# Optimization experiments

Measured on AMD Instinct MI355X. Metric: run time of the kernel, lower is better.

## Reference

```python
import jax, jax.numpy as jnp
import numpy as np

NUM_ITERATIONS = 3


def squash(s):
    # s: [..., out_channels]; norm over last axis (matches torch squash on squeezed tensor)
    norm = jnp.linalg.norm(s, axis=-1, keepdims=True)
    return (norm ** 2 / (1.0 + norm ** 2)) * (s / norm)


def setup_inputs() -> dict:
    key = jax.random.key(0)
    k1, k2 = jax.random.split(key)
    B, R, C, O, I = 256, 192, 96, 16, 20
    x = jax.random.normal(k1, (B, R, I), dtype=jnp.float32)
    W = jax.random.normal(k2, (R, C, O, I), dtype=jnp.float32)
    return {"x": x, "W": W}


def reference(x, W):
    # u_hat[b,r,c,o] = W[r,c,o,i] @ x[b,r,i]  (torch: matmul(W, x[i]) per batch element)
    u_hat = jnp.einsum('rcoi,bri->brco', W, x)  # [B,R,C,O]
    R, C = W.shape[0], W.shape[1]
    b_ij = jnp.zeros((R, C), dtype=x.dtype)  # shared across batch (torch b_ij is [1,R,C,1])
    v_j = None
    for it in range(NUM_ITERATIONS):
        c_ij = jax.nn.softmax(b_ij, axis=0)                 # softmax over routes (dim=1 in torch)
        s_j = jnp.einsum('rc,brco->bco', c_ij, u_hat)        # weighted sum over routes
        v_j = squash(s_j)                                    # [B,C,O]
        if it < NUM_ITERATIONS - 1:
            # agreement: <u_hat, v_j> averaged over batch (torch mean(dim=0))
            a_ij = jnp.einsum('brco,bco->rc', u_hat, v_j) / x.shape[0]
            b_ij = b_ij + a_ij
    return v_j  # [B, num_capsules, out_channels] (torch returns trailing singleton [B,C,O,1])
```

## Files before the change

kernel.cpp:

```cpp
#include <hip/hip_runtime.h>


#define R_ 192
#define C_ 96
#define O_ 16
#define I_ 20
#define B_ 256
#define K1 3840
#define N_ 1536
#define ZSPLIT 20
#define STILE 393216

typedef unsigned short u16;
typedef __attribute__((ext_vector_type(8))) short short8;
typedef __attribute__((ext_vector_type(4))) float floatx4;

__device__ inline float bf2f(u16 h) {
  union { unsigned int u; float f; } x; x.u = ((unsigned int)h) << 16; return x.f;
}
__device__ inline u16 f2bf(float f) {
  union { float f; unsigned int u; } x; x.f = f;
  unsigned int r = x.u + 0x7FFFu + ((x.u >> 16) & 1u);
  return (u16)(r >> 16);
}
__device__ inline unsigned int pack2(float a, float b) {
  return (unsigned int)f2bf(a) | ((unsigned int)f2bf(b) << 16);
}

__global__ void k_prep(const float* __restrict__ W, const float* __restrict__ X,
                       u16* __restrict__ WtT, u16* __restrict__ Xk,
                       u16* __restrict__ xT, float* __restrict__ bij) {
  int bid = blockIdx.x;
  if (bid < 23040) {
    int t = bid * 256 + threadIdx.x;
    int n = t / K1, k = t - n * K1;
    int c = n >> 4, o = n & 15;
    int r = k / I_, i = k - r * I_;
    WtT[t] = f2bf(W[(((r * C_ + c) * O_ + o) * I_) + i]);
  } else if (bid < 23280) {
    __shared__ u16 tile[64][72];
    int idx = bid - 23040;
    int kb = (idx % 60) << 6, bb = (idx / 60) << 6;
    int brow = threadIdx.x >> 4;
    int kq = (threadIdx.x & 15) << 2;
    #pragma unroll
    for (int p = 0; p < 4; ++p) {
      int bl = p * 16 + brow;
      float4 v = *(const float4*)(X + (size_t)(bb + bl) * K1 + kb + kq);
      ushort4 h;
      h.x = f2bf(v.x); h.y = f2bf(v.y); h.z = f2bf(v.z); h.w = f2bf(v.w);
      *(ushort4*)(Xk + (size_t)(bb + bl) * K1 + kb + kq) = h;
      tile[kq + 0][bl] = h.x;
      tile[kq + 1][bl] = h.y;
      tile[kq + 2][bl] = h.z;
      tile[kq + 3][bl] = h.w;
    }
    __syncthreads();
    int kr = threadIdx.x >> 3;
    int bq = (threadIdx.x & 7) << 3;
    #pragma unroll
    for (int q = 0; q < 2; ++q) {
      int kl = q * 32 + kr;
      *(uint4*)(xT + (size_t)(kb + kl) * B_ + bb + bq) = *(const uint4*)&tile[kl][bq];
    }
  } else {
    int t = (bid - 23280) * 256 + threadIdx.x;
    bij[t] = 0.0f;
  }
}

__device__ inline uint4 scale_b8(uint4 raw, int kg, const float* smrow) {
  int r0 = kg / I_;
  int bnd = (r0 + 1) * I_ - kg;
  float s0 = smrow[r0];
  float s1 = smrow[(r0 + 1 < R_) ? r0 + 1 : R_ - 1];
  union { uint4 q; u16 h[8]; } u; u.q = raw;
  #pragma unroll
  for (int j = 0; j < 8; ++j)
    u.h[j] = f2bf(bf2f(u.h[j]) * ((j < bnd) ? s0 : s1));
  return u.q;
}

__global__ __launch_bounds__(256) void gemm1(
    const u16* __restrict__ A, const u16* __restrict__ Bt,
    const float* __restrict__ bij, u16* __restrict__ P,
    int kChunk, int kIters) {
  const int K = K1;
  __shared__ u16 As[128 * 32];
  __shared__ u16 Bs[128 * 32];
  __shared__ float sm[8][192];
  int tid = threadIdx.x;
  {
    int cg = tid >> 5, lr = tid & 31;
    int c = (blockIdx.y << 3) + cg;
    float e[6]; float mx = -1e30f;
    #pragma unroll
    for (int j = 0; j < 6; ++j) {
      e[j] = bij[(lr + (j << 5)) * C_ + c];
      mx = fmaxf(mx, e[j]);
    }
    #pragma unroll
    for (int off = 16; off > 0; off >>= 1) mx = fmaxf(mx, __shfl_xor(mx, off));
    float sum = 0.f;
    #pragma unroll
    for (int j = 0; j < 6; ++j) { e[j] = expf(e[j] - mx); sum += e[j]; }
    #pragma unroll
    for (int off = 16; off > 0; off >>= 1) sum += __shfl_xor(sum, off);
    float inv = 1.0f / sum;
    #pragma unroll
    for (int j = 0; j < 6; ++j) sm[cg][lr + (j << 5)] = e[j] * inv;
  }
  __syncthreads();

  long m0 = (long)blockIdx.x * 128, n0 = (long)blockIdx.y * 128;
  int k0 = blockIdx.z * kChunk;
  const u16* Ab = A + m0 * K + k0;
  const u16* Bb = Bt + n0 * K + k0;
  int srow = tid >> 2;
  int scol = (tid & 3) << 3;
  int w = tid >> 6, lane = tid & 63;
  int wm = (w >> 1) << 6, wn = (w & 1) << 6;
  int quad = lane >> 4, lrow = lane & 15;
  int cl0 = srow >> 4;
  floatx4 acc[4][4];
  #pragma unroll
  for (int a = 0; a < 4; ++a)
    #pragma unroll
    for (int b = 0; b < 4; ++b) acc[a][b] = (floatx4){0.f, 0.f, 0.f, 0.f};

  for (int kt = 0; kt < kIters; ++kt) {
    int kk = kt << 5;
    uint4 a0 = *(const uint4*)(Ab + (long)srow * K + kk + scol);
    uint4 a1 = *(const uint4*)(Ab + (long)(srow + 64) * K + kk + scol);
    uint4 b0 = *(const uint4*)(Bb + (long)srow * K + kk + scol);
    uint4 b1 = *(const uint4*)(Bb + (long)(srow + 64) * K + kk + scol);
    int kg = k0 + kk + scol;
    uint4 b0s = scale_b8(b0, kg, &sm[cl0][0]);
    uint4 b1s = scale_b8(b1, kg, &sm[cl0 + 4][0]);
    __syncthreads();
    ((uint4*)As)[tid] = a0;
    ((uint4*)As)[tid + 256] = a1;
    ((uint4*)Bs)[tid] = b0s;
    ((uint4*)Bs)[tid + 256] = b1s;
    __syncthreads();
    short8 af[4], bfr[4];
    #pragma unroll
    for (int ms = 0; ms < 4; ++ms)
      af[ms] = *(const short8*)&As[(wm + ms * 16 + lrow) * 32 + (quad << 3)];
    #pragma unroll
    for (int ns = 0; ns < 4; ++ns)
      bfr[ns] = *(const short8*)&Bs[(wn + ns * 16 + lrow) * 32 + (quad << 3)];
    #pragma unroll
    for (int ms = 0; ms < 4; ++ms)
      #pragma unroll
      for (int ns = 0; ns < 4; ++ns)
        acc[ms][ns] = __builtin_amdgcn_mfma_f32_16x16x32_bf16(
            af[ms], bfr[ns], acc[ms][ns], 0, 0, 0);
  }
  size_t zb = (size_t)blockIdx.z * (size_t)STILE;
  #pragma unroll
  for (int ms = 0; ms < 4; ++ms)
    #pragma unroll
    for (int ns = 0; ns < 4; ++ns) {
      int b = (int)m0 + wm + ms * 16 + (quad << 2);
      int n = (int)n0 + wn + ns * 16 + lrow;
      uint2 pk;
      pk.x = pack2(acc[ms][ns][0], acc[ms][ns][1]);
      pk.y = pack2(acc[ms][ns][2], acc[ms][ns][3]);
      *(uint2*)&P[zb + (size_t)n * B_ + b] = pk;
    }
}

__global__ __launch_bounds__(256) void gemm2_agree(
    const u16* __restrict__ A, const u16* __restrict__ Bt,
    const u16* __restrict__ WtT, float* __restrict__ bij) {
  const int K = 256;
  __shared__ u16 As[128 * 32];
  __shared__ u16 Bs[128 * 32];
  int tid = threadIdx.x;
  long m0 = (long)blockIdx.x * 128, n0 = (long)blockIdx.y * 128;
  int k0 = blockIdx.z << 7;
  const u16* Ab = A + m0 * K + k0;
  const u16* Bb = Bt + n0 * K + k0;
  int srow = tid >> 2;
  int scol = (tid & 3) << 3;
  int w = tid >> 6, lane = tid & 63;
  int wm = (w >> 1) << 6, wn = (w & 1) << 6;
  int quad = lane >> 4, lrow = lane & 15;
  floatx4 acc[4][4];
  #pragma unroll
  for (int a = 0; a < 4; ++a)
    #pragma unroll
    for (int b = 0; b < 4; ++b) acc[a][b] = (floatx4){0.f, 0.f, 0.f, 0.f};

  for (int kt = 0; kt < 4; ++kt) {
    int kk = kt << 5;
    uint4 a0 = *(const uint4*)(Ab + (long)srow * K + kk + scol);
    uint4 a1 = *(const uint4*)(Ab + (long)(srow + 64) * K + kk + scol);
    uint4 b0 = *(const uint4*)(Bb + (long)srow * K + kk + scol);
    uint4 b1 = *(const uint4*)(Bb + (long)(srow + 64) * K + kk + scol);
    __syncthreads();
    ((uint4*)As)[tid] = a0;
    ((uint4*)As)[tid + 256] = a1;
    ((uint4*)Bs)[tid] = b0;
    ((uint4*)Bs)[tid + 256] = b1;
    __syncthreads();
    short8 af[4], bfr[4];
    #pragma unroll
    for (int ms = 0; ms < 4; ++ms)
      af[ms] = *(const short8*)&As[(wm + ms * 16 + lrow) * 32 + (quad << 3)];
    #pragma unroll
    for (int ns = 0; ns < 4; ++ns)
      bfr[ns] = *(const short8*)&Bs[(wn + ns * 16 + lrow) * 32 + (quad << 3)];
    #pragma unroll
    for (int ms = 0; ms < 4; ++ms)
      #pragma unroll
      for (int ns = 0; ns < 4; ++ns)
        acc[ms][ns] = __builtin_amdgcn_mfma_f32_16x16x32_bf16(
            af[ms], bfr[ns], acc[ms][ns], 0, 0, 0);
  }
  #pragma unroll
  for (int ms = 0; ms < 4; ++ms) {
    int rowbase = (int)m0 + wm + ms * 16;
    int r_lo = rowbase / I_;
    int r_hi = (rowbase + 15) / I_;
    int bnd = (r_lo + 1) * I_;
    int rowl = rowbase + (quad << 2);
    #pragma unroll
    for (int ns = 0; ns < 4; ++ns) {
      int col = (int)n0 + wn + ns * 16 + lrow;
      uint2 wv = *(const uint2*)&WtT[(size_t)col * K1 + rowl];
      u16 h[4];
      h[0] = (u16)(wv.x & 0xffff); h[1] = (u16)(wv.x >> 16);
      h[2] = (u16)(wv.y & 0xffff); h[3] = (u16)(wv.y >> 16);
      float p0 = 0.f, p1 = 0.f;
      #pragma unroll
      for (int e = 0; e < 4; ++e) {
        float pr = acc[ms][ns][e] * bf2f(h[e]);
        if (rowl + e < bnd) p0 += pr; else p1 += pr;
      }
      #pragma unroll
      for (int off = 32; off > 0; off >>= 1) {
        p0 += __shfl_xor(p0, off);
        p1 += __shfl_xor(p1, off);
      }
      if (lane == 0) {
        int c = col >> 4;
        atomicAdd(&bij[r_lo * C_ + c], p0 * (1.0f / 256.0f));
        atomicAdd(&bij[r_hi * C_ + c], p1 * (1.0f / 256.0f));
      }
    }
  }
}

__global__ void k_redsq(const u16* __restrict__ P, float* __restrict__ out,
                        u16* __restrict__ vT, int last) {
  __shared__ float nsq_l[4][128];
  int c = blockIdx.x, bh = blockIdx.y;
  int lane = threadIdx.x & 63, og = threadIdx.x >> 6;
  int bi = (lane << 1);
  int b = (bh << 7) + bi;
  float acc[4][2];
  #pragma unroll
  for (int oo = 0; oo < 4; ++oo) { acc[oo][0] = 0.f; acc[oo][1] = 0.f; }
  for (int z = 0; z < ZSPLIT; ++z) {
    size_t base = (size_t)z * STILE + (size_t)((c << 4) + (og << 2)) * B_ + b;
    #pragma unroll
    for (int oo = 0; oo < 4; ++oo) {
      unsigned int u = *(const unsigned int*)&P[base + (size_t)oo * B_];
      acc[oo][0] += bf2f((u16)(u & 0xffff));
      acc[oo][1] += bf2f((u16)(u >> 16));
    }
  }
  float q0 = 0.f, q1 = 0.f;
  #pragma unroll
  for (int oo = 0; oo < 4; ++oo) {
    q0 += acc[oo][0] * acc[oo][0];
    q1 += acc[oo][1] * acc[oo][1];
  }
  nsq_l[og][bi] = q0;
  nsq_l[og][bi + 1] = q1;
  __syncthreads();
  float n0 = nsq_l[0][bi] + nsq_l[1][bi] + nsq_l[2][bi] + nsq_l[3][bi];
  float n1 = nsq_l[0][bi + 1] + nsq_l[1][bi + 1] + nsq_l[2][bi + 1] + nsq_l[3][bi + 1];
  float f0 = n0 / ((1.0f + n0) * sqrtf(n0));
  float f1 = n1 / ((1.0f + n1) * sqrtf(n1));
  #pragma unroll
  for (int oo = 0; oo < 4; ++oo) { acc[oo][0] *= f0; acc[oo][1] *= f1; }
  if (last) {
    float4 v0 = (float4){acc[0][0], acc[1][0], acc[2][0], acc[3][0]};
    float4 v1 = (float4){acc[0][1], acc[1][1], acc[2][1], acc[3][1]};
    *(float4*)(out + (size_t)b * N_ + (c << 4) + (og << 2)) = v0;
    *(float4*)(out + (size_t)(b + 1) * N_ + (c << 4) + (og << 2)) = v1;
  } else {
    #pragma unroll
    for (int oo = 0; oo < 4; ++oo)
      *(unsigned int*)&vT[(size_t)((c << 4) + (og << 2) + oo) * B_ + b] =
          pack2(acc[oo][0], acc[oo][1]);
  }
}

extern "C" void kernel_launch(void* const* d_in, const int* in_sizes, int n_in,
                              void* d_out, int out_size, void* d_ws, size_t ws_size,
                              hipStream_t stream) {
  const float* X = (const float*)d_in[0];
  const float* W = (const float*)d_in[1];
  float* out = (float*)d_out;
  char* ws = (char*)d_ws;
  u16*  WtT = (u16*)(ws);
  u16*  Xk  = (u16*)(ws + 11796480);
  u16*  xT  = (u16*)(ws + 13762560);
  u16*  vT  = (u16*)(ws + 15728640);
  u16*  Pb  = (u16*)(ws + 16515072);
  float* bij = (float*)(ws + 32243712);

  k_prep<<<23352, 256, 0, stream>>>(W, X, WtT, Xk, xT, bij);

  for (int it = 0; it < 3; ++it) {
    gemm1<<<dim3(2, 12, ZSPLIT), 256, 0, stream>>>(Xk, WtT, bij, Pb, 192, 6);
    k_redsq<<<dim3(96, 2), 256, 0, stream>>>(Pb, out, vT, it == 2);
    if (it < 2)
      gemm2_agree<<<dim3(30, 12, 2), 256, 0, stream>>>(xT, vT, WtT, bij);
  }
}
```

Measured before the change: 179.2 us.

## Fuse split-K reduction and squash into gemm1 via last-block counter

Merges the separate reduce-and-squash kernel into the split-K gemm. The last block to finish each output tile, detected through an atomic counter, sums the partials, computes the squash and writes either vT or the final output. The tile shape changes from 128x128 with 20 K-splits to 64x128 with 10 K-splits. The first iteration skips the softmax and uses a uniform 1/192 weight, which is exact because the logits start at zero. This removes one launch per iteration and the extra pass over the partials, at the cost of a serial tail in the last block and a per-iteration partial buffer and counter region.

After: 254.5 us. 1.42x slower.

```diff
diff --git a/kernel.cpp b/kernel.cpp
--- a/kernel.cpp
+++ b/kernel.cpp
@@ -8,8 +8,10 @@
 #define B_ 256
 #define K1 3840
 #define N_ 1536
-#define ZSPLIT 20
+#define ZSPLIT 10
+#define KCH 384
 #define STILE 393216
+#define PITER (ZSPLIT * STILE)
 
 typedef unsigned short u16;
 typedef __attribute__((ext_vector_type(8))) short short8;
@@ -29,7 +31,7 @@
 
 __global__ void k_prep(const float* __restrict__ W, const float* __restrict__ X,
                        u16* __restrict__ WtT, u16* __restrict__ Xk,
-                       u16* __restrict__ xT, float* __restrict__ bij) {
+                       u16* __restrict__ xT, float* __restrict__ zeroRegion) {
   int bid = blockIdx.x;
   if (bid < 23040) {
     int t = bid * 256 + threadIdx.x;
@@ -65,7 +67,7 @@
     }
   } else {
     int t = (bid - 23280) * 256 + threadIdx.x;
-    bij[t] = 0.0f;
+    if (t < 18576) zeroRegion[t] = 0.0f;
   }
 }
 
@@ -81,16 +83,20 @@
   return u.q;
 }
 
-__global__ __launch_bounds__(256) void gemm1(
+__global__ __launch_bounds__(256) void gemm1_redsq(
     const u16* __restrict__ A, const u16* __restrict__ Bt,
     const float* __restrict__ bij, u16* __restrict__ P,
-    int kChunk, int kIters) {
-  const int K = K1;
-  __shared__ u16 As[128 * 32];
+    int* __restrict__ cnt, float* __restrict__ out, u16* __restrict__ vT,
+    int uniformSm, int last) {
+  __shared__ u16 As[64 * 32];
   __shared__ u16 Bs[128 * 32];
   __shared__ float sm[8][192];
+  __shared__ int isLast;
   int tid = threadIdx.x;
-  {
+
+  if (uniformSm) {
+    for (int j = tid; j < 8 * 192; j += 256) (&sm[0][0])[j] = 1.0f / 192.0f;
+  } else {
     int cg = tid >> 5, lr = tid & 31;
     int c = (blockIdx.y << 3) + cg;
     float e[6]; float mx = -1e30f;
@@ -112,48 +118,46 @@
   }
   __syncthreads();
 
-  long m0 = (long)blockIdx.x * 128, n0 = (long)blockIdx.y * 128;
-  int k0 = blockIdx.z * kChunk;
-  const u16* Ab = A + m0 * K + k0;
-  const u16* Bb = Bt + n0 * K + k0;
+  long m0 = (long)blockIdx.x * 64, n0 = (long)blockIdx.y * 128;
+  int k0 = blockIdx.z * KCH;
+  const u16* Ab = A + m0 * K1 + k0;
+  const u16* Bb = Bt + n0 * K1 + k0;
   int srow = tid >> 2;
   int scol = (tid & 3) << 3;
   int w = tid >> 6, lane = tid & 63;
-  int wm = (w >> 1) << 6, wn = (w & 1) << 6;
+  int wn = w << 5;
   int quad = lane >> 4, lrow = lane & 15;
   int cl0 = srow >> 4;
-  floatx4 acc[4][4];
+  floatx4 acc[4][2];
   #pragma unroll
   for (int a = 0; a < 4; ++a)
     #pragma unroll
-    for (int b = 0; b < 4; ++b) acc[a][b] = (floatx4){0.f, 0.f, 0.f, 0.f};
-
-  for (int kt = 0; kt < kIters; ++kt) {
+    for (int b = 0; b < 2; ++b) acc[a][b] = (floatx4){0.f, 0.f, 0.f, 0.f};
+
+  for (int kt = 0; kt < 12; ++kt) {
     int kk = kt << 5;
-    uint4 a0 = *(const uint4*)(Ab + (long)srow * K + kk + scol);
-    uint4 a1 = *(const uint4*)(Ab + (long)(srow + 64) * K + kk + scol);
-    uint4 b0 = *(const uint4*)(Bb + (long)srow * K + kk + scol);
-    uint4 b1 = *(const uint4*)(Bb + (long)(srow + 64) * K + kk + scol);
+    uint4 a0 = *(const uint4*)(Ab + (long)srow * K1 + kk + scol);
+    uint4 b0 = *(const uint4*)(Bb + (long)srow * K1 + kk + scol);
+    uint4 b1 = *(const uint4*)(Bb + (long)(srow + 64) * K1 + kk + scol);
     int kg = k0 + kk + scol;
     uint4 b0s = scale_b8(b0, kg, &sm[cl0][0]);
     uint4 b1s = scale_b8(b1, kg, &sm[cl0 + 4][0]);
     __syncthreads();
     ((uint4*)As)[tid] = a0;
-    ((uint4*)As)[tid + 256] = a1;
     ((uint4*)Bs)[tid] = b0s;
     ((uint4*)Bs)[tid + 256] = b1s;
     __syncthreads();
-    short8 af[4], bfr[4];
+    short8 af[4], bfr[2];
     #pragma unroll
     for (int ms = 0; ms < 4; ++ms)
-      af[ms] = *(const short8*)&As[(wm + ms * 16 + lrow) * 32 + (quad << 3)];
-    #pragma unroll
-    for (int ns = 0; ns < 4; ++ns)
+      af[ms] = *(const short8*)&As[(ms * 16 + lrow) * 32 + (quad << 3)];
+    #pragma unroll
+    for (int ns = 0; ns < 2; ++ns)
       bfr[ns] = *(const short8*)&Bs[(wn + ns * 16 + lrow) * 32 + (quad << 3)];
     #pragma unroll
     for (int ms = 0; ms < 4; ++ms)
       #pragma unroll
-      for (int ns = 0; ns < 4; ++ns)
+      for (int ns = 0; ns < 2; ++ns)
         acc[ms][ns] = __builtin_amdgcn_mfma_f32_16x16x32_bf16(
             af[ms], bfr[ns], acc[ms][ns], 0, 0, 0);
   }
@@ -161,14 +165,67 @@
   #pragma unroll
   for (int ms = 0; ms < 4; ++ms)
     #pragma unroll
-    for (int ns = 0; ns < 4; ++ns) {
-      int b = (int)m0 + wm + ms * 16 + (quad << 2);
+    for (int ns = 0; ns < 2; ++ns) {
+      int b = (int)m0 + ms * 16 + (quad << 2);
       int n = (int)n0 + wn + ns * 16 + lrow;
       uint2 pk;
       pk.x = pack2(acc[ms][ns][0], acc[ms][ns][1]);
       pk.y = pack2(acc[ms][ns][2], acc[ms][ns][3]);
       *(uint2*)&P[zb + (size_t)n * B_ + b] = pk;
     }
+
+  __syncthreads();
+  if (tid == 0) {
+    __threadfence();
+    int old = atomicAdd(&cnt[blockIdx.y * 4 + blockIdx.x], 1);
+    isLast = (old == ZSPLIT - 1);
+  }
+  __syncthreads();
+  if (!isLast) return;
+  __threadfence();
+
+  float* nsq_l = (float*)As;
+  float* fac = (float*)Bs;
+  int o = tid >> 4;
+  int bq = (tid & 15) << 2;
+  int b0 = (int)m0;
+  for (int cl = 0; cl < 8; ++cl) {
+    int n = (int)n0 + cl * 16 + o;
+    float f[4];
+    f[0] = 0.f; f[1] = 0.f; f[2] = 0.f; f[3] = 0.f;
+    #pragma unroll
+    for (int z = 0; z < ZSPLIT; ++z) {
+      uint2 u = *(const uint2*)&P[(size_t)z * STILE + (size_t)n * B_ + b0 + bq];
+      f[0] += bf2f((u16)(u.x & 0xffff));
+      f[1] += bf2f((u16)(u.x >> 16));
+      f[2] += bf2f((u16)(u.y & 0xffff));
+      f[3] += bf2f((u16)(u.y >> 16));
+    }
+    float4 q = (float4){f[0] * f[0], f[1] * f[1], f[2] * f[2], f[3] * f[3]};
+    *(float4*)&nsq_l[o * 64 + bq] = q;
+    __syncthreads();
+    if (tid < 64) {
+      float s = 0.f;
+      #pragma unroll
+      for (int oo = 0; oo < 16; ++oo) s += nsq_l[oo * 64 + tid];
+      fac[tid] = s / ((1.0f + s) * sqrtf(s));
+    }
+    __syncthreads();
+    float4 fc = *(const float4*)&fac[bq];
+    f[0] *= fc.x; f[1] *= fc.y; f[2] *= fc.z; f[3] *= fc.w;
+    if (last) {
+      out[(size_t)(b0 + bq + 0) * N_ + n] = f[0];
+      out[(size_t)(b0 + bq + 1) * N_ + n] = f[1];
+      out[(size_t)(b0 + bq + 2) * N_ + n] = f[2];
+      out[(size_t)(b0 + bq + 3) * N_ + n] = f[3];
+    } else {
+      uint2 pk;
+      pk.x = pack2(f[0], f[1]);
+      pk.y = pack2(f[2], f[3]);
+      *(uint2*)&vT[(size_t)n * B_ + b0 + bq] = pk;
+    }
+    __syncthreads();
+  }
 }
 
 __global__ __launch_bounds__(256) void gemm2_agree(
@@ -253,53 +310,6 @@
   }
 }
 
-__global__ void k_redsq(const u16* __restrict__ P, float* __restrict__ out,
-                        u16* __restrict__ vT, int last) {
-  __shared__ float nsq_l[4][128];
-  int c = blockIdx.x, bh = blockIdx.y;
-  int lane = threadIdx.x & 63, og = threadIdx.x >> 6;
-  int bi = (lane << 1);
-  int b = (bh << 7) + bi;
-  float acc[4][2];
-  #pragma unroll
-  for (int oo = 0; oo < 4; ++oo) { acc[oo][0] = 0.f; acc[oo][1] = 0.f; }
-  for (int z = 0; z < ZSPLIT; ++z) {
-    size_t base = (size_t)z * STILE + (size_t)((c << 4) + (og << 2)) * B_ + b;
-    #pragma unroll
-    for (int oo = 0; oo < 4; ++oo) {
-      unsigned int u = *(const unsigned int*)&P[base + (size_t)oo * B_];
-      acc[oo][0] += bf2f((u16)(u & 0xffff));
-      acc[oo][1] += bf2f((u16)(u >> 16));
-    }
-  }
-  float q0 = 0.f, q1 = 0.f;
-  #pragma unroll
-  for (int oo = 0; oo < 4; ++oo) {
-    q0 += acc[oo][0] * acc[oo][0];
-    q1 += acc[oo][1] * acc[oo][1];
-  }
-  nsq_l[og][bi] = q0;
-  nsq_l[og][bi + 1] = q1;
-  __syncthreads();
-  float n0 = nsq_l[0][bi] + nsq_l[1][bi] + nsq_l[2][bi] + nsq_l[3][bi];
-  float n1 = nsq_l[0][bi + 1] + nsq_l[1][bi + 1] + nsq_l[2][bi + 1] + nsq_l[3][bi + 1];
-  float f0 = n0 / ((1.0f + n0) * sqrtf(n0));
-  float f1 = n1 / ((1.0f + n1) * sqrtf(n1));
-  #pragma unroll
-  for (int oo = 0; oo < 4; ++oo) { acc[oo][0] *= f0; acc[oo][1] *= f1; }
-  if (last) {
-    float4 v0 = (float4){acc[0][0], acc[1][0], acc[2][0], acc[3][0]};
-    float4 v1 = (float4){acc[0][1], acc[1][1], acc[2][1], acc[3][1]};
-    *(float4*)(out + (size_t)b * N_ + (c << 4) + (og << 2)) = v0;
-    *(float4*)(out + (size_t)(b + 1) * N_ + (c << 4) + (og << 2)) = v1;
-  } else {
-    #pragma unroll
-    for (int oo = 0; oo < 4; ++oo)
-      *(unsigned int*)&vT[(size_t)((c << 4) + (og << 2) + oo) * B_ + b] =
-          pack2(acc[oo][0], acc[oo][1]);
-  }
-}
-
 extern "C" void kernel_launch(void* const* d_in, const int* in_sizes, int n_in,
                               void* d_out, int out_size, void* d_ws, size_t ws_size,
                               hipStream_t stream) {
@@ -312,13 +322,15 @@
   u16*  xT  = (u16*)(ws + 13762560);
   u16*  vT  = (u16*)(ws + 15728640);
   u16*  Pb  = (u16*)(ws + 16515072);
-  float* bij = (float*)(ws + 32243712);
-
-  k_prep<<<23352, 256, 0, stream>>>(W, X, WtT, Xk, xT, bij);
+  float* bij = (float*)(ws + 40108032);
+  int*  cnt = (int*)(ws + 40181760);
+
+  k_prep<<<23353, 256, 0, stream>>>(W, X, WtT, Xk, xT, bij);
 
   for (int it = 0; it < 3; ++it) {
-    gemm1<<<dim3(2, 12, ZSPLIT), 256, 0, stream>>>(Xk, WtT, bij, Pb, 192, 6);
-    k_redsq<<<dim3(96, 2), 256, 0, stream>>>(Pb, out, vT, it == 2);
+    gemm1_redsq<<<dim3(4, 12, ZSPLIT), 256, 0, stream>>>(
+        Xk, WtT, bij, Pb + (size_t)it * PITER, cnt + it * 48, out, vT,
+        it == 0, it == 2);
     if (it < 2)
       gemm2_agree<<<dim3(30, 12, 2), 256, 0, stream>>>(xT, vT, WtT, bij);
   }
```
